# Kernel optimization log

Measured on AMD Instinct MI355X. Metric: run time of the kernel, lower is better.

The kernel has to match this reference:

```python
import jax, jax.numpy as jnp
import numpy as np
from jax import lax

C_IN = 256
P = 4
S_D = 512
N_GROUPS = C_IN // P          # 64
C_OUT = C_IN                  # 256
CIN_G = C_IN // N_GROUPS      # 4 (in-channels per group, depthwise stage)
COUT_G = C_OUT // N_GROUPS    # 4 (channels per group, pointwise stage)
EPS = 1e-5


def setup_inputs() -> dict:
    key = jax.random.key(0)
    ks = jax.random.split(key, 8)
    style_encoding = jax.random.normal(ks[0], (8, S_D, 4, 4), dtype=jnp.float32)
    predicted = jax.random.normal(ks[1], (8, C_IN, 128, 128), dtype=jnp.float32)
    # kernel-generator parameters (xavier-ish scale)
    dw_w = jax.random.normal(ks[2], (C_OUT * CIN_G, S_D, 2, 2), dtype=jnp.float32) * 0.03
    dw_b = jnp.full((C_OUT * CIN_G,), 0.01, dtype=jnp.float32)
    pw_kn_w = jax.random.normal(ks[3], (C_OUT * COUT_G, S_D, 1, 1), dtype=jnp.float32) * 0.05
    pw_kn_b = jnp.full((C_OUT * COUT_G,), 0.01, dtype=jnp.float32)
    pw_b_w = jax.random.normal(ks[4], (C_OUT, S_D, 1, 1), dtype=jnp.float32) * 0.05
    pw_b_b = jnp.full((C_OUT,), 0.01, dtype=jnp.float32)
    return {"style_encoding": style_encoding, "predicted": predicted,
            "dw_w": dw_w, "dw_b": dw_b, "pw_kn_w": pw_kn_w, "pw_kn_b": pw_kn_b,
            "pw_b_w": pw_b_w, "pw_b_b": pw_b_b}


def reference(style_encoding, predicted, dw_w, dw_b, pw_kn_w, pw_kn_b, pw_b_w, pw_b_b):
    N = style_encoding.shape[0]
    # --- generate per-sample depthwise 3x3 grouped-conv kernels ---
    dw = lax.conv_general_dilated(style_encoding, dw_w, (1, 1), 'VALID',
                                  dimension_numbers=('NCHW', 'OIHW', 'NCHW'))
    dw = dw + dw_b[None, :, None, None]                 # [N, C_OUT*CIN_G, 3, 3]
    dw = dw.reshape(N, C_OUT, CIN_G, 3, 3)
    # --- double 2x2 avg pool on 4x4 style == global spatial mean ---
    s = jnp.mean(style_encoding, axis=(2, 3))           # [N, S_D]
    # 1x1 convs on 1x1 maps == linear layers
    pw_kn = (s @ pw_kn_w.reshape(C_OUT * COUT_G, S_D).T + pw_kn_b)
    pw_kn = pw_kn.reshape(N, N_GROUPS, COUT_G, COUT_G)  # [N, g, out/g, in/g]
    pw_bias = s @ pw_b_w.reshape(C_OUT, S_D).T + pw_b_b  # [N, C_OUT]
    # --- instance norm (no affine) on content features ---
    mean = predicted.mean(axis=(2, 3), keepdims=True)
    x = predicted - mean
    x = x * lax.rsqrt(jnp.mean(jnp.square(x), axis=(2, 3), keepdims=True) + EPS)
    # --- reflection pad (1,1,1,1) ---
    x = jnp.pad(x, ((0, 0), (0, 0), (1, 1), (1, 1)), mode='reflect')
    # --- per-sample grouped 3x3 conv, vectorized over batch via vmap ---
    def conv_one(xi, wi):
        return lax.conv_general_dilated(xi[None], wi, (1, 1), 'VALID',
                                        dimension_numbers=('NCHW', 'OIHW', 'NCHW'),
                                        feature_group_count=N_GROUPS)[0]
    y = jax.vmap(conv_one)(x, dw)                       # [N, C_OUT, H, W]
    # --- per-sample grouped 1x1 conv as a batched group einsum ---
    H, W = y.shape[2], y.shape[3]
    yg = y.reshape(N, N_GROUPS, COUT_G, H, W)
    out = jnp.einsum('ngihw,ngoi->ngohw', yg, pw_kn).reshape(N, C_OUT, H, W)
    out = out + pw_bias[:, :, None, None]
    return out
```

## Files before the change

### kernel.cpp

```cpp
#include <hip/hip_runtime.h>

#define NB 8
#define SD 512
#define HW 128
#define EPS 1e-5f

__device__ __forceinline__ int refl(int r) { return r < 0 ? 1 : (r > 127 ? 126 : r); }

__global__ __launch_bounds__(256) void prep_k(const float* __restrict__ pred,
                                              const float* __restrict__ style,
                                              const float* __restrict__ dww,
                                              const float* __restrict__ dwb,
                                              float* __restrict__ dw_ws,
                                              float* __restrict__ mean_ws,
                                              float* __restrict__ inv_ws) {
    __shared__ float ws4[4], wss4[4];
    int b = blockIdx.x, t = threadIdx.x;
    int q = b >> 1;
    if ((b & 1) == 0) {
        const float4* p = (const float4*)(pred + (size_t)q * HW * HW);
        float s = 0.f, ss = 0.f;
#pragma unroll
        for (int k = 0; k < 16; ++k) {
            float4 v = p[k * 256 + t];
            s  += v.x + v.y + v.z + v.w;
            ss += v.x * v.x + v.y * v.y + v.z * v.z + v.w * v.w;
        }
#pragma unroll
        for (int off = 32; off; off >>= 1) {
            s  += __shfl_down(s, off);
            ss += __shfl_down(ss, off);
        }
        if ((t & 63) == 0) { ws4[t >> 6] = s; wss4[t >> 6] = ss; }
        __syncthreads();
        if (t == 0) {
            float S  = ws4[0] + ws4[1] + ws4[2] + ws4[3];
            float SS = wss4[0] + wss4[1] + wss4[2] + wss4[3];
            float m = S * (1.f / (HW * HW));
            float var = SS * (1.f / (HW * HW)) - m * m;
            mean_ws[q] = m;
            inv_ws[q] = rsqrtf(var + EPS);
        }
    } else {
        int n = q & 7;
        int f = ((q >> 3) << 2) + (t >> 6);
        int lane = t & 63;
        float acc[9];
#pragma unroll
        for (int k = 0; k < 9; ++k) acc[k] = 0.f;
#pragma unroll 2
        for (int it = 0; it < 8; ++it) {
            int c = lane + (it << 6);
            const float4* sp = (const float4*)(style + ((size_t)n * SD + c) * 16);
            float st[16];
#pragma unroll
            for (int k = 0; k < 4; ++k) {
                float4 v = sp[k];
                st[k * 4 + 0] = v.x; st[k * 4 + 1] = v.y;
                st[k * 4 + 2] = v.z; st[k * 4 + 3] = v.w;
            }
            float4 w = *(const float4*)(dww + ((size_t)f * SD + c) * 4);
#pragma unroll
            for (int p = 0; p < 3; ++p)
#pragma unroll
                for (int qq = 0; qq < 3; ++qq)
                    acc[p * 3 + qq] += st[p * 4 + qq] * w.x + st[p * 4 + qq + 1] * w.y
                                     + st[(p + 1) * 4 + qq] * w.z + st[(p + 1) * 4 + qq + 1] * w.w;
        }
#pragma unroll
        for (int k = 0; k < 9; ++k)
#pragma unroll
            for (int off = 32; off; off >>= 1) acc[k] += __shfl_down(acc[k], off);
        if (lane == 0) {
            float bias = dwb[f];
#pragma unroll
            for (int k = 0; k < 9; ++k)
                dw_ws[((size_t)n * 1024 + f) * 9 + k] = acc[k] + bias;
        }
    }
}

__global__ __launch_bounds__(256) void fold2_k(const float* __restrict__ style,
                                               const float* __restrict__ pkw,
                                               const float* __restrict__ pkb,
                                               const float* __restrict__ pbw,
                                               const float* __restrict__ pbb,
                                               const float* __restrict__ mean_ws,
                                               const float* __restrict__ inv_ws,
                                               float* __restrict__ dw_ws,
                                               float* __restrict__ pwb_ws) {
    __shared__ float s_lds[SD];
    __shared__ float dwl[144], pwkl[16], invl[4], msc[4], pwbl[4];
    int b = blockIdx.x;
    int n = b >> 6, g = b & 63;
    int t = threadIdx.x;
    size_t dbase = (size_t)(n * 64 + g) * 144;

    if (t < 144) dwl[t] = dw_ws[dbase + t];
    else if (t < 148) {
        int ic = t - 144;
        float m = mean_ws[n * 256 + g * 4 + ic];
        float s = inv_ws[n * 256 + g * 4 + ic];
        invl[ic] = s; msc[ic] = m * s;
    }
#pragma unroll
    for (int c0 = 0; c0 < 2; ++c0) {
        int c = t + (c0 << 8);
        const float4* sp = (const float4*)(style + ((size_t)n * SD + c) * 16);
        float4 a0 = sp[0], a1 = sp[1], a2 = sp[2], a3 = sp[3];
        float sum = a0.x + a0.y + a0.z + a0.w + a1.x + a1.y + a1.z + a1.w
                  + a2.x + a2.y + a2.z + a2.w + a3.x + a3.y + a3.z + a3.w;
        s_lds[c] = sum * (1.f / 16.f);
    }
    __syncthreads();

    int wv = t >> 6, lane = t & 63;
#pragma unroll
    for (int qd = 0; qd < 5; ++qd) {
        int u = wv * 5 + qd;
        const float2* wrow = (const float2*)((u < 16)
                              ? (pkw + (size_t)(g * 16 + u) * SD)
                              : (pbw + (size_t)(g * 4 + (u - 16)) * SD));
        float a = 0.f;
#pragma unroll
        for (int it = 0; it < 4; ++it) {
            int c2 = lane + (it << 6);
            float2 x = ((const float2*)s_lds)[c2];
            float2 v = wrow[c2];
            a += x.x * v.x + x.y * v.y;
        }
#pragma unroll
        for (int off = 32; off; off >>= 1) a += __shfl_down(a, off);
        if (lane == 0) {
            if (u < 16) pwkl[u] = a + pkb[g * 16 + u];
            else        pwbl[u - 16] = a + pbb[g * 4 + (u - 16)];
        }
    }
    __syncthreads();

    if (t < 144) {
        int o = t / 36, rm = t % 36, ic = rm / 9, k = rm % 9;
        int kh = k / 3, kw = k % 3;
        float a = 0.f;
#pragma unroll
        for (int i = 0; i < 4; ++i) a += pwkl[o * 4 + i] * dwl[(i * 4 + ic) * 9 + k];
        dw_ws[dbase + (size_t)(((ic * 3 + kh) * 3 + kw) * 4 + o)] = a * invl[ic];
    } else if (t < 148) {
        int o = t - 144;
        float cb = 0.f;
#pragma unroll
        for (int i = 0; i < 4; ++i) {
            float s2 = 0.f;
#pragma unroll
            for (int ic = 0; ic < 4; ++ic) {
                float sk = 0.f;
#pragma unroll
                for (int k = 0; k < 9; ++k) sk += dwl[(i * 4 + ic) * 9 + k];
                s2 += msc[ic] * sk;
            }
            cb += pwkl[o * 4 + i] * s2;
        }
        pwb_ws[n * 256 + g * 4 + o] = pwbl[o] - cb;
    }
}

__global__ __launch_bounds__(256) void adaconv_main_k(const float* __restrict__ pred,
                                                      const float* __restrict__ Wf,
                                                      const float* __restrict__ Bf,
                                                      float* __restrict__ out) {
    int b = blockIdx.x;
    int strip = b & 7;
    int g = (b >> 3) & 63;
    int n = b >> 9;
    int t = threadIdx.x;
    const size_t gbase = (size_t)(n * 64 + g);
    const size_t cbase = (size_t)(n * 256 + g * 4);
    int row2 = t >> 5;
    int colq = t & 31;
    int lane = t & 63;
    int r0 = (strip << 4) + (row2 << 1);
    int wr0 = refl(r0 - 1), wr3 = refl(r0 + 2);

    const float* Wp = Wf + gbase * 144;
    const float* Bp = Bf + gbase * 4;

    float4 v[4][4];
#pragma unroll
    for (int ic = 0; ic < 4; ++ic) {
        const float* pc = pred + (cbase + ic) * (HW * HW) + (colq << 2);
        v[ic][0] = *(const float4*)(pc + wr0 * HW);
        v[ic][1] = *(const float4*)(pc + (size_t)r0 * HW);
        v[ic][2] = *(const float4*)(pc + (size_t)(r0 + 1) * HW);
        v[ic][3] = *(const float4*)(pc + wr3 * HW);
    }

    float acc[2][4][4];
#pragma unroll
    for (int o = 0; o < 4; ++o) {
        float bb = Bp[o];
#pragma unroll
        for (int p = 0; p < 4; ++p) { acc[0][o][p] = bb; acc[1][o][p] = bb; }
    }

#pragma unroll
    for (int ic = 0; ic < 4; ++ic) {
#pragma unroll
        for (int wr = 0; wr < 4; ++wr) {
            float4 vv = v[ic][wr];
            float lw = __shfl(vv.w, lane - 1);
            float rx = __shfl(vv.x, lane + 1);
            float e0 = (colq == 0)  ? vv.y : lw;
            float e5 = (colq == 31) ? vv.z : rx;
            float e[6] = {e0, vv.x, vv.y, vv.z, vv.w, e5};
#pragma unroll
            for (int ro = 0; ro < 2; ++ro) {
                int kh = wr - ro;
                if (kh < 0 || kh > 2) continue;
                const float* wp = Wp + (ic * 3 + kh) * 12;
#pragma unroll
                for (int kw = 0; kw < 3; ++kw) {
                    float w0 = wp[kw * 4 + 0], w1 = wp[kw * 4 + 1];
                    float w2 = wp[kw * 4 + 2], w3 = wp[kw * 4 + 3];
#pragma unroll
                    for (int p = 0; p < 4; ++p) {
                        acc[ro][0][p] = fmaf(w0, e[p + kw], acc[ro][0][p]);
                        acc[ro][1][p] = fmaf(w1, e[p + kw], acc[ro][1][p]);
                        acc[ro][2][p] = fmaf(w2, e[p + kw], acc[ro][2][p]);
                        acc[ro][3][p] = fmaf(w3, e[p + kw], acc[ro][3][p]);
                    }
                }
            }
        }
    }

#pragma unroll
    for (int ro = 0; ro < 2; ++ro)
#pragma unroll
        for (int o = 0; o < 4; ++o) {
            *(float4*)(out + (cbase + o) * (HW * HW) + (size_t)(r0 + ro) * HW + (colq << 2)) =
                make_float4(acc[ro][o][0], acc[ro][o][1], acc[ro][o][2], acc[ro][o][3]);
        }
}

extern "C" void kernel_launch(void* const* d_in, const int* in_sizes, int n_in,
                              void* d_out, int out_size, void* d_ws, size_t ws_size,
                              hipStream_t stream) {
    const float* style = (const float*)d_in[0];
    const float* pred  = (const float*)d_in[1];
    const float* dww   = (const float*)d_in[2];
    const float* dwb   = (const float*)d_in[3];
    const float* pkw   = (const float*)d_in[4];
    const float* pkb   = (const float*)d_in[5];
    const float* pbw   = (const float*)d_in[6];
    const float* pbb   = (const float*)d_in[7];
    float* out = (float*)d_out;

    float* ws      = (float*)d_ws;
    float* dw_ws   = ws + 4096;
    float* pwb_ws  = ws + 86016;
    float* mean_ws = ws + 88064;
    float* inv_ws  = ws + 90112;

    prep_k<<<4096, 256, 0, stream>>>(pred, style, dww, dwb, dw_ws, mean_ws, inv_ws);
    fold2_k<<<NB * 64, 256, 0, stream>>>(style, pkw, pkb, pbw, pbb,
                                         mean_ws, inv_ws, dw_ws, pwb_ws);
    adaconv_main_k<<<4096, 256, 0, stream>>>(pred, dw_ws, pwb_ws, out);
}
```

Measured before the change: 95.55 us.

## Fuse style-kernel generation and folding into prep; apply instance-norm in main kernel

Merges the separate fold kernel into the prep kernel. Each block of five now handles either a channel's statistics or a whole (n,g) weight record, with 16 depthwise filters per block instead of 4. Because the statistics are no longer ready when weights are folded, the per-channel inv-std scaling and mean-derived bias correction move into the main conv kernel, which multiplies inputs by inv-std and computes the bias from stored row sums. This removes one launch and its grid-wide dependency, at the cost of extra per-element multiplies in the main kernel and a longer serial filter loop per block.

```diff
diff --git a/kernel.cpp b/kernel.cpp
--- a/kernel.cpp
+++ b/kernel.cpp
@@ -4,21 +4,27 @@
 #define SD 512
 #define HW 128
 #define EPS 1e-5f
+#define WREC 164
 
 __device__ __forceinline__ int refl(int r) { return r < 0 ? 1 : (r > 127 ? 126 : r); }
 
-__global__ __launch_bounds__(256) void prep_k(const float* __restrict__ pred,
-                                              const float* __restrict__ style,
-                                              const float* __restrict__ dww,
-                                              const float* __restrict__ dwb,
-                                              float* __restrict__ dw_ws,
-                                              float* __restrict__ mean_ws,
-                                              float* __restrict__ inv_ws) {
-    __shared__ float ws4[4], wss4[4];
+__global__ __launch_bounds__(256) void prep2_k(const float* __restrict__ pred,
+                                               const float* __restrict__ style,
+                                               const float* __restrict__ dww,
+                                               const float* __restrict__ dwb,
+                                               const float* __restrict__ pkw,
+                                               const float* __restrict__ pkb,
+                                               const float* __restrict__ pbw,
+                                               const float* __restrict__ pbb,
+                                               float* __restrict__ wrec,
+                                               float* __restrict__ mean_ws,
+                                               float* __restrict__ inv_ws) {
     int b = blockIdx.x, t = threadIdx.x;
-    int q = b >> 1;
-    if ((b & 1) == 0) {
-        const float4* p = (const float4*)(pred + (size_t)q * HW * HW);
+    int q5 = b / 5, r5 = b - q5 * 5;
+    if (r5 < 4) {
+        __shared__ float ws4[4], wss4[4];
+        int c = q5 * 4 + r5;
+        const float4* p = (const float4*)(pred + (size_t)c * HW * HW);
         float s = 0.f, ss = 0.f;
 #pragma unroll
         for (int k = 0; k < 16; ++k) {
@@ -38,142 +44,124 @@
             float SS = wss4[0] + wss4[1] + wss4[2] + wss4[3];
             float m = S * (1.f / (HW * HW));
             float var = SS * (1.f / (HW * HW)) - m * m;
-            mean_ws[q] = m;
-            inv_ws[q] = rsqrtf(var + EPS);
+            mean_ws[c] = m;
+            inv_ws[c] = rsqrtf(var + EPS);
         }
     } else {
-        int n = q & 7;
-        int f = ((q >> 3) << 2) + (t >> 6);
-        int lane = t & 63;
-        float acc[9];
-#pragma unroll
-        for (int k = 0; k < 9; ++k) acc[k] = 0.f;
+        __shared__ float s_lds[SD];
+        __shared__ float dwl[144];
+        __shared__ float pwkl[16], pwbl[4];
+        int u = q5;
+        int n = u & 7;
+        int g = u >> 3;
+        int wv = t >> 6, lane = t & 63;
+
+#pragma unroll
+        for (int c0 = 0; c0 < 2; ++c0) {
+            int c = t + (c0 << 8);
+            const float4* sp = (const float4*)(style + ((size_t)n * SD + c) * 16);
+            float4 a0 = sp[0], a1 = sp[1], a2 = sp[2], a3 = sp[3];
+            float sum = a0.x + a0.y + a0.z + a0.w + a1.x + a1.y + a1.z + a1.w
+                      + a2.x + a2.y + a2.z + a2.w + a3.x + a3.y + a3.z + a3.w;
+            s_lds[c] = sum * (1.f / 16.f);
+        }
+
+#pragma unroll
+        for (int rep = 0; rep < 4; ++rep) {
+            int fl = wv * 4 + rep;
+            int f = g * 16 + fl;
+            float acc[9];
+#pragma unroll
+            for (int k = 0; k < 9; ++k) acc[k] = 0.f;
 #pragma unroll 2
-        for (int it = 0; it < 8; ++it) {
-            int c = lane + (it << 6);
-            const float4* sp = (const float4*)(style + ((size_t)n * SD + c) * 16);
-            float st[16];
-#pragma unroll
-            for (int k = 0; k < 4; ++k) {
-                float4 v = sp[k];
-                st[k * 4 + 0] = v.x; st[k * 4 + 1] = v.y;
-                st[k * 4 + 2] = v.z; st[k * 4 + 3] = v.w;
-            }
-            float4 w = *(const float4*)(dww + ((size_t)f * SD + c) * 4);
-#pragma unroll
-            for (int p = 0; p < 3; ++p)
-#pragma unroll
-                for (int qq = 0; qq < 3; ++qq)
-                    acc[p * 3 + qq] += st[p * 4 + qq] * w.x + st[p * 4 + qq + 1] * w.y
-                                     + st[(p + 1) * 4 + qq] * w.z + st[(p + 1) * 4 + qq + 1] * w.w;
-        }
-#pragma unroll
-        for (int k = 0; k < 9; ++k)
-#pragma unroll
-            for (int off = 32; off; off >>= 1) acc[k] += __shfl_down(acc[k], off);
-        if (lane == 0) {
-            float bias = dwb[f];
+            for (int it = 0; it < 8; ++it) {
+                int c = lane + (it << 6);
+                const float4* sp = (const float4*)(style + ((size_t)n * SD + c) * 16);
+                float st[16];
+#pragma unroll
+                for (int k = 0; k < 4; ++k) {
+                    float4 v = sp[k];
+                    st[k * 4 + 0] = v.x; st[k * 4 + 1] = v.y;
+                    st[k * 4 + 2] = v.z; st[k * 4 + 3] = v.w;
+                }
+                float4 w = *(const float4*)(dww + ((size_t)f * SD + c) * 4);
+#pragma unroll
+                for (int p = 0; p < 3; ++p)
+#pragma unroll
+                    for (int qq = 0; qq < 3; ++qq)
+                        acc[p * 3 + qq] += st[p * 4 + qq] * w.x + st[p * 4 + qq + 1] * w.y
+                                         + st[(p + 1) * 4 + qq] * w.z + st[(p + 1) * 4 + qq + 1] * w.w;
+            }
 #pragma unroll
             for (int k = 0; k < 9; ++k)
-                dw_ws[((size_t)n * 1024 + f) * 9 + k] = acc[k] + bias;
+#pragma unroll
+                for (int off = 32; off; off >>= 1) acc[k] += __shfl_down(acc[k], off);
+            if (lane == 0) {
+                float bias = dwb[f];
+#pragma unroll
+                for (int k = 0; k < 9; ++k) dwl[fl * 9 + k] = acc[k] + bias;
+            }
+        }
+        __syncthreads();
+
+#pragma unroll
+        for (int qd = 0; qd < 5; ++qd) {
+            int u20 = wv * 5 + qd;
+            const float2* wrow = (const float2*)((u20 < 16)
+                                  ? (pkw + (size_t)(g * 16 + u20) * SD)
+                                  : (pbw + (size_t)(g * 4 + (u20 - 16)) * SD));
+            float a = 0.f;
+#pragma unroll
+            for (int it = 0; it < 4; ++it) {
+                int c2 = lane + (it << 6);
+                float2 x = ((const float2*)s_lds)[c2];
+                float2 v = wrow[c2];
+                a += x.x * v.x + x.y * v.y;
+            }
+#pragma unroll
+            for (int off = 32; off; off >>= 1) a += __shfl_down(a, off);
+            if (lane == 0) {
+                if (u20 < 16) pwkl[u20] = a + pkb[g * 16 + u20];
+                else          pwbl[u20 - 16] = a + pbb[g * 4 + (u20 - 16)];
+            }
+        }
+        __syncthreads();
+
+        float* wr = wrec + (size_t)u * WREC;
+        if (t < 144) {
+            int o = t / 36, rm = t % 36, ic = rm / 9, k = rm % 9;
+            int kh = k / 3, kw = k % 3;
+            float a = 0.f;
+#pragma unroll
+            for (int i = 0; i < 4; ++i) a += pwkl[o * 4 + i] * dwl[(i * 4 + ic) * 9 + k];
+            wr[((ic * 3 + kh) * 3 + kw) * 4 + o] = a;
+        } else if (t < 160) {
+            int j = t - 144, o = j >> 2, ic = j & 3;
+            float a = 0.f;
+#pragma unroll
+            for (int i = 0; i < 4; ++i) {
+                float sk = 0.f;
+#pragma unroll
+                for (int k = 0; k < 9; ++k) sk += dwl[(i * 4 + ic) * 9 + k];
+                a += pwkl[o * 4 + i] * sk;
+            }
+            wr[144 + j] = a;
+        } else if (t < 164) {
+            wr[160 + (t - 160)] = pwbl[t - 160];
         }
     }
 }
 
-__global__ __launch_bounds__(256) void fold2_k(const float* __restrict__ style,
-                                               const float* __restrict__ pkw,
-                                               const float* __restrict__ pkb,
-                                               const float* __restrict__ pbw,
-                                               const float* __restrict__ pbb,
-                                               const float* __restrict__ mean_ws,
-                                               const float* __restrict__ inv_ws,
-                                               float* __restrict__ dw_ws,
-                                               float* __restrict__ pwb_ws) {
-    __shared__ float s_lds[SD];
-    __shared__ float dwl[144], pwkl[16], invl[4], msc[4], pwbl[4];
-    int b = blockIdx.x;
-    int n = b >> 6, g = b & 63;
-    int t = threadIdx.x;
-    size_t dbase = (size_t)(n * 64 + g) * 144;
-
-    if (t < 144) dwl[t] = dw_ws[dbase + t];
-    else if (t < 148) {
-        int ic = t - 144;
-        float m = mean_ws[n * 256 + g * 4 + ic];
-        float s = inv_ws[n * 256 + g * 4 + ic];
-        invl[ic] = s; msc[ic] = m * s;
-    }
-#pragma unroll
-    for (int c0 = 0; c0 < 2; ++c0) {
-        int c = t + (c0 << 8);
-        const float4* sp = (const float4*)(style + ((size_t)n * SD + c) * 16);
-        float4 a0 = sp[0], a1 = sp[1], a2 = sp[2], a3 = sp[3];
-        float sum = a0.x + a0.y + a0.z + a0.w + a1.x + a1.y + a1.z + a1.w
-                  + a2.x + a2.y + a2.z + a2.w + a3.x + a3.y + a3.z + a3.w;
-        s_lds[c] = sum * (1.f / 16.f);
-    }
-    __syncthreads();
-
-    int wv = t >> 6, lane = t & 63;
-#pragma unroll
-    for (int qd = 0; qd < 5; ++qd) {
-        int u = wv * 5 + qd;
-        const float2* wrow = (const float2*)((u < 16)
-                              ? (pkw + (size_t)(g * 16 + u) * SD)
-                              : (pbw + (size_t)(g * 4 + (u - 16)) * SD));
-        float a = 0.f;
-#pragma unroll
-        for (int it = 0; it < 4; ++it) {
-            int c2 = lane + (it << 6);
-            float2 x = ((const float2*)s_lds)[c2];
-            float2 v = wrow[c2];
-            a += x.x * v.x + x.y * v.y;
-        }
-#pragma unroll
-        for (int off = 32; off; off >>= 1) a += __shfl_down(a, off);
-        if (lane == 0) {
-            if (u < 16) pwkl[u] = a + pkb[g * 16 + u];
-            else        pwbl[u - 16] = a + pbb[g * 4 + (u - 16)];
-        }
-    }
-    __syncthreads();
-
-    if (t < 144) {
-        int o = t / 36, rm = t % 36, ic = rm / 9, k = rm % 9;
-        int kh = k / 3, kw = k % 3;
-        float a = 0.f;
-#pragma unroll
-        for (int i = 0; i < 4; ++i) a += pwkl[o * 4 + i] * dwl[(i * 4 + ic) * 9 + k];
-        dw_ws[dbase + (size_t)(((ic * 3 + kh) * 3 + kw) * 4 + o)] = a * invl[ic];
-    } else if (t < 148) {
-        int o = t - 144;
-        float cb = 0.f;
-#pragma unroll
-        for (int i = 0; i < 4; ++i) {
-            float s2 = 0.f;
-#pragma unroll
-            for (int ic = 0; ic < 4; ++ic) {
-                float sk = 0.f;
-#pragma unroll
-                for (int k = 0; k < 9; ++k) sk += dwl[(i * 4 + ic) * 9 + k];
-                s2 += msc[ic] * sk;
-            }
-            cb += pwkl[o * 4 + i] * s2;
-        }
-        pwb_ws[n * 256 + g * 4 + o] = pwbl[o] - cb;
-    }
-}
-
 __global__ __launch_bounds__(256) void adaconv_main_k(const float* __restrict__ pred,
-                                                      const float* __restrict__ Wf,
-                                                      const float* __restrict__ Bf,
+                                                      const float* __restrict__ wrec,
+                                                      const float* __restrict__ meanv,
+                                                      const float* __restrict__ invv,
                                                       float* __restrict__ out) {
     int b = blockIdx.x;
     int strip = b & 7;
     int g = (b >> 3) & 63;
     int n = b >> 9;
     int t = threadIdx.x;
-    const size_t gbase = (size_t)(n * 64 + g);
     const size_t cbase = (size_t)(n * 256 + g * 4);
     int row2 = t >> 5;
     int colq = t & 31;
@@ -181,8 +169,11 @@
     int r0 = (strip << 4) + (row2 << 1);
     int wr0 = refl(r0 - 1), wr3 = refl(r0 + 2);
 
-    const float* Wp = Wf + gbase * 144;
-    const float* Bp = Bf + gbase * 4;
+    const float* Wp = wrec + (size_t)(g * 8 + n) * WREC;
+    float inv0 = invv[cbase + 0], inv1 = invv[cbase + 1];
+    float inv2 = invv[cbase + 2], inv3 = invv[cbase + 3];
+    float msc0 = meanv[cbase + 0] * inv0, msc1 = meanv[cbase + 1] * inv1;
+    float msc2 = meanv[cbase + 2] * inv2, msc3 = meanv[cbase + 3] * inv3;
 
     float4 v[4][4];
 #pragma unroll
@@ -197,16 +188,20 @@
     float acc[2][4][4];
 #pragma unroll
     for (int o = 0; o < 4; ++o) {
-        float bb = Bp[o];
+        float bb = Wp[160 + o]
+                 - msc0 * Wp[144 + o * 4 + 0] - msc1 * Wp[144 + o * 4 + 1]
+                 - msc2 * Wp[144 + o * 4 + 2] - msc3 * Wp[144 + o * 4 + 3];
 #pragma unroll
         for (int p = 0; p < 4; ++p) { acc[0][o][p] = bb; acc[1][o][p] = bb; }
     }
 
 #pragma unroll
     for (int ic = 0; ic < 4; ++ic) {
+        float sc = ic == 0 ? inv0 : (ic == 1 ? inv1 : (ic == 2 ? inv2 : inv3));
 #pragma unroll
         for (int wr = 0; wr < 4; ++wr) {
             float4 vv = v[ic][wr];
+            vv.x *= sc; vv.y *= sc; vv.z *= sc; vv.w *= sc;
             float lw = __shfl(vv.w, lane - 1);
             float rx = __shfl(vv.x, lane + 1);
             float e0 = (colq == 0)  ? vv.y : lw;
@@ -256,13 +251,11 @@
     float* out = (float*)d_out;
 
     float* ws      = (float*)d_ws;
-    float* dw_ws   = ws + 4096;
-    float* pwb_ws  = ws + 86016;
-    float* mean_ws = ws + 88064;
-    float* inv_ws  = ws + 90112;
-
-    prep_k<<<4096, 256, 0, stream>>>(pred, style, dww, dwb, dw_ws, mean_ws, inv_ws);
-    fold2_k<<<NB * 64, 256, 0, stream>>>(style, pkw, pkb, pbw, pbb,
-                                         mean_ws, inv_ws, dw_ws, pwb_ws);
-    adaconv_main_k<<<4096, 256, 0, stream>>>(pred, dw_ws, pwb_ws, out);
+    float* wrec_ws = ws;
+    float* mean_ws = ws + 83968;
+    float* inv_ws  = ws + 86016;
+
+    prep2_k<<<2560, 256, 0, stream>>>(pred, style, dww, dwb, pkw, pkb, pbw, pbb,
+                                      wrec_ws, mean_ws, inv_ws);
+    adaconv_main_k<<<4096, 256, 0, stream>>>(pred, wrec_ws, mean_ws, inv_ws, out);
 }
```

After: 105.4 us. 1.1x slower.
